# Performance work log

Hardware: AMD Instinct MI355X
Metric: run time of the kernel (lower is better)

## Reference

```python
import jax, jax.numpy as jnp
import numpy as np

B, C, T, N, KS = 16, 64, 64, 1024, 3

def setup_inputs() -> dict:
    key = jax.random.key(0)
    k1, k2, k3, k4 = jax.random.split(key, 4)
    x = jax.random.normal(k1, (B, C, T, N), dtype=jnp.float32)
    # scaled Chebyshev Laplacian terms; scale keeps activations sane
    Lk = jax.random.normal(k2, (KS, N, N), dtype=jnp.float32) / np.sqrt(N)
    # kaiming-uniform-ish init: bound = sqrt(6 / fan_in), fan_in = C*KS
    fan_in = C * KS
    bound_t = float(np.sqrt(6.0 / fan_in))
    theta = jax.random.uniform(k3, (C, C, KS), dtype=jnp.float32, minval=-bound_t, maxval=bound_t)
    bound_b = float(1.0 / np.sqrt(fan_in))
    b = jax.random.uniform(k4, (1, C, 1, 1), dtype=jnp.float32, minval=-bound_b, maxval=bound_b)
    return {"x": x, "Lk": Lk, "theta": theta, "b": b}

def reference(x, Lk, theta, b):
    # x: [b, c, t, n]; Lk: [ks, n, n]; theta: [c_in, c_out, ks]; b: [1, c, 1, 1]
    # Chebyshev graph contraction: aggregate over source nodes m for each order k
    x_c = jnp.einsum('knm,bitm->bitkn', Lk, x)          # [b, c, t, ks, n]
    # channel mixing over (c_in, ks)
    x_gc = jnp.einsum('iok,bitkn->botn', theta, x_c) + b  # [b, c, t, n]
    return jax.nn.relu(x_gc + x)
```

## Files before the change

### kernel.cpp

```cpp
#include <hip/hip_runtime.h>
#include <cstdint>
#include <cstddef>

typedef unsigned short u16;
typedef __attribute__((ext_vector_type(8))) short short8;
typedef __attribute__((ext_vector_type(4))) float f32x4;

#define B_DIM 16
#define C_DIM 64
#define T_DIM 64
#define N_DIM 1024
#define KS_DIM 3

#define BN 128
#define BK 32
#define NSTEP (N_DIM / BK)

__device__ __forceinline__ u16 f2bf(float f) {
  union { float f; uint32_t u; } v; v.f = f;
  uint32_t r = (v.u + 0x7FFFu + ((v.u >> 16) & 1u)) >> 16;
  return (u16)r;
}

__device__ __forceinline__ void gload_lds16(const void* g, void* l) {
  __builtin_amdgcn_global_load_lds(
      (const __attribute__((address_space(1))) void*)g,
      (__attribute__((address_space(3))) void*)l, 16, 0, 0);
}

__global__ void k_convert_lk(const float* __restrict__ Lk, u16* __restrict__ Lkb) {
  size_t idx = (size_t)blockIdx.x * blockDim.x + threadIdx.x;
  const float4* s = (const float4*)(Lk + idx * 8);
  float4 f0 = s[0], f1 = s[1];
  short8 h;
  h[0] = (short)f2bf(f0.x); h[1] = (short)f2bf(f0.y);
  h[2] = (short)f2bf(f0.z); h[3] = (short)f2bf(f0.w);
  h[4] = (short)f2bf(f1.x); h[5] = (short)f2bf(f1.y);
  h[6] = (short)f2bf(f1.z); h[7] = (short)f2bf(f1.w);
  *(short8*)(Lkb + idx * 8) = h;
}

__global__ void k_convert_theta(const float* __restrict__ th, u16* __restrict__ thT) {
  int f = blockIdx.x * blockDim.x + threadIdx.x;
  if (f < C_DIM * C_DIM * KS_DIM) {
    int o = f / 192, ik = f % 192, k = ik >> 6, i = ik & 63;
    thT[f] = f2bf(th[(i * 64 + o) * 3 + k]);
  }
}

__global__ __launch_bounds__(256, 3)
void k_main(const float* __restrict__ x, const u16* __restrict__ Lkb,
            const u16* __restrict__ thT, const float* __restrict__ bias,
            float* __restrict__ out) {
  __shared__ __align__(16) char smem[51200];
  u16* Ab = (u16*)smem;
  u16* Bb = (u16*)(smem + 4096);
  char* Zb = smem;

  const int tid = threadIdx.x;
  const int wv = tid >> 6;
  const int ln = tid & 63;
  const int lg = ln >> 4;
  const int l16 = ln & 15;

  const int bid = blockIdx.x;
  const int nt = bid & 7;
  const int slice = bid >> 3;
  const int bb = slice >> 6;
  const int tti = slice & 63;

  const f32x4 vzero = {0.f, 0.f, 0.f, 0.f};
  f32x4 acc[4][6];
#pragma unroll
  for (int a = 0; a < 4; ++a)
#pragma unroll
    for (int c = 0; c < 6; ++c) acc[a][c] = vzero;

  const int arow = tid >> 2, am = tid & 3;
  const float* a_src = x + (((size_t)bb * C_DIM + arow) * T_DIM + tti) * N_DIM + am * 8;

  for (int kk = 0; kk < NSTEP; ++kk) {
    if (kk) __syncthreads();
    {
      const float4* s = (const float4*)(a_src + kk * BK);
      float4 f0 = s[0], f1 = s[1];
      short8 h;
      h[0] = (short)f2bf(f0.x); h[1] = (short)f2bf(f0.y);
      h[2] = (short)f2bf(f0.z); h[3] = (short)f2bf(f0.w);
      h[4] = (short)f2bf(f1.x); h[5] = (short)f2bf(f1.y);
      h[6] = (short)f2bf(f1.z); h[7] = (short)f2bf(f1.w);
      *(short8*)(Ab + arow * BK + am * 8) = h;
    }
#pragma unroll
    for (int it = 0; it < 6; ++it) {
      int L = it * 256 + tid;
      int brow = L >> 2, msub = L & 3;
      int k = brow >> 7, nl = brow & 127;
      const u16* src = Lkb + ((size_t)(k * N_DIM + nt * BN + nl)) * N_DIM + kk * BK + msub * 8;
      char* dst = (char*)Bb + (size_t)(it * 256 + wv * 64) * 16;
      gload_lds16(src, dst);
    }
    __syncthreads();
    short8 af[4];
#pragma unroll
    for (int mi = 0; mi < 4; ++mi)
      af[mi] = *(const short8*)(Ab + (mi * 16 + l16) * BK + lg * 8);
#pragma unroll
    for (int ci = 0; ci < 6; ++ci) {
      int r = wv * 96 + ci * 16 + l16;
      short8 bf = *(const short8*)(Bb + r * BK + lg * 8);
#pragma unroll
      for (int mi = 0; mi < 4; ++mi)
        acc[mi][ci] = __builtin_amdgcn_mfma_f32_16x16x32_bf16(af[mi], bf, acc[mi][ci], 0, 0, 0);
    }
  }

  __syncthreads();
#pragma unroll
  for (int mi = 0; mi < 4; ++mi)
#pragma unroll
    for (int ci = 0; ci < 6; ++ci) {
      int c = wv * 96 + ci * 16 + l16;
      int k = c >> 7, nl = c & 127;
      int ib = mi * 16 + lg * 4;
      uint32_t p0 = (uint32_t)f2bf(acc[mi][ci][0]) | ((uint32_t)f2bf(acc[mi][ci][1]) << 16);
      uint32_t p1 = (uint32_t)f2bf(acc[mi][ci][2]) | ((uint32_t)f2bf(acc[mi][ci][3]) << 16);
      *(uint32_t*)(Zb + ((size_t)nl * 200 + k * 64 + ib) * 2) = p0;
      *(uint32_t*)(Zb + ((size_t)nl * 200 + k * 64 + ib + 2) * 2) = p1;
    }
  __syncthreads();

  f32x4 acc2[4][2];
#pragma unroll
  for (int a = 0; a < 4; ++a)
#pragma unroll
    for (int c = 0; c < 2; ++c) acc2[a][c] = vzero;

#pragma unroll
  for (int ks = 0; ks < 6; ++ks) {
    short8 af2[4];
#pragma unroll
    for (int mo = 0; mo < 4; ++mo) {
      int o = mo * 16 + l16;
      af2[mo] = *(const short8*)(thT + o * 192 + ks * 32 + lg * 8);
    }
#pragma unroll
    for (int cj = 0; cj < 2; ++cj) {
      int nl = wv * 32 + cj * 16 + l16;
      short8 bf = *(const short8*)(Zb + ((size_t)nl * 200 + ks * 32 + lg * 8) * 2);
#pragma unroll
      for (int mo = 0; mo < 4; ++mo)
        acc2[mo][cj] = __builtin_amdgcn_mfma_f32_16x16x32_bf16(af2[mo], bf, acc2[mo][cj], 0, 0, 0);
    }
  }

#pragma unroll
  for (int mo = 0; mo < 4; ++mo)
#pragma unroll
    for (int cj = 0; cj < 2; ++cj) {
      int nl = wv * 32 + cj * 16 + l16;
      int n = nt * BN + nl;
#pragma unroll
      for (int r = 0; r < 4; ++r) {
        int o = mo * 16 + lg * 4 + r;
        size_t oi = (((size_t)bb * C_DIM + o) * T_DIM + tti) * N_DIM + n;
        float v = acc2[mo][cj][r] + bias[o] + x[oi];
        out[oi] = v > 0.f ? v : 0.f;
      }
    }
}

extern "C" void kernel_launch(void* const* d_in, const int* in_sizes, int n_in,
                              void* d_out, int out_size, void* d_ws, size_t ws_size,
                              hipStream_t stream) {
  (void)in_sizes; (void)n_in; (void)out_size; (void)ws_size;
  const float* x     = (const float*)d_in[0];
  const float* Lk    = (const float*)d_in[1];
  const float* theta = (const float*)d_in[2];
  const float* bias  = (const float*)d_in[3];
  float* out = (float*)d_out;

  u16* Lkb = (u16*)d_ws;
  u16* thT = (u16*)((char*)d_ws + (size_t)KS_DIM * N_DIM * N_DIM * 2);

  k_convert_lk<<<KS_DIM * N_DIM * N_DIM / 8 / 256, 256, 0, stream>>>(Lk, Lkb);
  k_convert_theta<<<(C_DIM * C_DIM * KS_DIM + 255) / 256, 256, 0, stream>>>(theta, thT);
  k_main<<<B_DIM * T_DIM * (N_DIM / BN), 256, 0, stream>>>(x, Lkb, thT, bias, out);
}
```

Before: 1.020 ms.

## Double-buffer Lk tiles in LDS and XOR-swizzle A/B shared layouts

Moves the Lk (B) tile into two LDS buffers so the next k-step's async global-to-LDS loads are issued before the current step's MFMAs, overlapping memory with compute. The x (A) tile's fp32 loads for the next step are prefetched into registers and converted and stored after a barrier. An XOR swizzle on the 16-byte column chunk is applied to both A and B tiles to reduce LDS bank conflicts on fragment reads. Shared memory grows to 52KB and a second barrier per iteration is added, which may limit occupancy against the 3-blocks launch bound.

```diff
diff --git a/kernel.cpp b/kernel.cpp
--- a/kernel.cpp
+++ b/kernel.cpp
@@ -52,9 +52,10 @@
 void k_main(const float* __restrict__ x, const u16* __restrict__ Lkb,
             const u16* __restrict__ thT, const float* __restrict__ bias,
             float* __restrict__ out) {
-  __shared__ __align__(16) char smem[51200];
-  u16* Ab = (u16*)smem;
-  u16* Bb = (u16*)(smem + 4096);
+  __shared__ __align__(16) char smem[53248];
+  u16* Bb0 = (u16*)smem;
+  u16* Bb1 = (u16*)(smem + 24576);
+  u16* Ab  = (u16*)(smem + 49152);
   char* Zb = smem;
 
   const int tid = threadIdx.x;
@@ -78,44 +79,71 @@
 
   const int arow = tid >> 2, am = tid & 3;
   const float* a_src = x + (((size_t)bb * C_DIM + arow) * T_DIM + tti) * N_DIM + am * 8;
+  u16* a_dst = Ab + arow * BK + ((am ^ ((arow >> 1) & 3)) << 3);
+
+  const u16* b_srcb[6];
+  char* b_dst_off[6];
+#pragma unroll
+  for (int it = 0; it < 6; ++it) {
+    int L = it * 256 + tid;
+    int brow = L >> 2, msub = L & 3;
+    int k = brow >> 7, nl = brow & 127;
+    int msw = msub ^ ((brow >> 1) & 3);
+    b_srcb[it] = Lkb + ((size_t)(k * N_DIM + nt * BN + nl)) * N_DIM + (msw << 3);
+    b_dst_off[it] = (char*)((size_t)(it * 256 + wv * 64) * 16);
+  }
+
+  float4 a0 = *(const float4*)(a_src);
+  float4 a1 = *(const float4*)(a_src + 4);
+#pragma unroll
+  for (int it = 0; it < 6; ++it)
+    gload_lds16(b_srcb[it], (char*)Bb0 + (size_t)b_dst_off[it]);
+  {
+    short8 h;
+    h[0] = (short)f2bf(a0.x); h[1] = (short)f2bf(a0.y);
+    h[2] = (short)f2bf(a0.z); h[3] = (short)f2bf(a0.w);
+    h[4] = (short)f2bf(a1.x); h[5] = (short)f2bf(a1.y);
+    h[6] = (short)f2bf(a1.z); h[7] = (short)f2bf(a1.w);
+    *(short8*)a_dst = h;
+  }
+  __syncthreads();
 
   for (int kk = 0; kk < NSTEP; ++kk) {
-    if (kk) __syncthreads();
-    {
-      const float4* s = (const float4*)(a_src + kk * BK);
-      float4 f0 = s[0], f1 = s[1];
-      short8 h;
-      h[0] = (short)f2bf(f0.x); h[1] = (short)f2bf(f0.y);
-      h[2] = (short)f2bf(f0.z); h[3] = (short)f2bf(f0.w);
-      h[4] = (short)f2bf(f1.x); h[5] = (short)f2bf(f1.y);
-      h[6] = (short)f2bf(f1.z); h[7] = (short)f2bf(f1.w);
-      *(short8*)(Ab + arow * BK + am * 8) = h;
-    }
-#pragma unroll
-    for (int it = 0; it < 6; ++it) {
-      int L = it * 256 + tid;
-      int brow = L >> 2, msub = L & 3;
-      int k = brow >> 7, nl = brow & 127;
-      const u16* src = Lkb + ((size_t)(k * N_DIM + nt * BN + nl)) * N_DIM + kk * BK + msub * 8;
-      char* dst = (char*)Bb + (size_t)(it * 256 + wv * 64) * 16;
-      gload_lds16(src, dst);
-    }
-    __syncthreads();
+    u16* Bcur = (kk & 1) ? Bb1 : Bb0;
+    u16* Bnxt = (kk & 1) ? Bb0 : Bb1;
+    if (kk + 1 < NSTEP) {
+#pragma unroll
+      for (int it = 0; it < 6; ++it)
+        gload_lds16(b_srcb[it] + (kk + 1) * BK, (char*)Bnxt + (size_t)b_dst_off[it]);
+      a0 = *(const float4*)(a_src + (kk + 1) * BK);
+      a1 = *(const float4*)(a_src + (kk + 1) * BK + 4);
+    }
     short8 af[4];
 #pragma unroll
-    for (int mi = 0; mi < 4; ++mi)
-      af[mi] = *(const short8*)(Ab + (mi * 16 + l16) * BK + lg * 8);
+    for (int mi = 0; mi < 4; ++mi) {
+      int row = mi * 16 + l16;
+      af[mi] = *(const short8*)(Ab + row * BK + ((lg ^ ((row >> 1) & 3)) << 3));
+    }
 #pragma unroll
     for (int ci = 0; ci < 6; ++ci) {
       int r = wv * 96 + ci * 16 + l16;
-      short8 bf = *(const short8*)(Bb + r * BK + lg * 8);
+      short8 bfr = *(const short8*)(Bcur + r * BK + ((lg ^ ((r >> 1) & 3)) << 3));
 #pragma unroll
       for (int mi = 0; mi < 4; ++mi)
-        acc[mi][ci] = __builtin_amdgcn_mfma_f32_16x16x32_bf16(af[mi], bf, acc[mi][ci], 0, 0, 0);
-    }
-  }
-
-  __syncthreads();
+        acc[mi][ci] = __builtin_amdgcn_mfma_f32_16x16x32_bf16(af[mi], bfr, acc[mi][ci], 0, 0, 0);
+    }
+    __syncthreads();
+    if (kk + 1 < NSTEP) {
+      short8 h;
+      h[0] = (short)f2bf(a0.x); h[1] = (short)f2bf(a0.y);
+      h[2] = (short)f2bf(a0.z); h[3] = (short)f2bf(a0.w);
+      h[4] = (short)f2bf(a1.x); h[5] = (short)f2bf(a1.y);
+      h[6] = (short)f2bf(a1.z); h[7] = (short)f2bf(a1.w);
+      *(short8*)a_dst = h;
+    }
+    __syncthreads();
+  }
+
 #pragma unroll
   for (int mi = 0; mi < 4; ++mi)
 #pragma unroll
@@ -147,10 +175,10 @@
 #pragma unroll
     for (int cj = 0; cj < 2; ++cj) {
       int nl = wv * 32 + cj * 16 + l16;
-      short8 bf = *(const short8*)(Zb + ((size_t)nl * 200 + ks * 32 + lg * 8) * 2);
+      short8 bfr = *(const short8*)(Zb + ((size_t)nl * 200 + ks * 32 + lg * 8) * 2);
 #pragma unroll
       for (int mo = 0; mo < 4; ++mo)
-        acc2[mo][cj] = __builtin_amdgcn_mfma_f32_16x16x32_bf16(af2[mo], bf, acc2[mo][cj], 0, 0, 0);
+        acc2[mo][cj] = __builtin_amdgcn_mfma_f32_16x16x32_bf16(af2[mo], bfr, acc2[mo][cj], 0, 0, 0);
     }
   }
 
```

Measured after the change: 1.011 ms. No clear change (-0.8%).

## Retile main GEMM to 256x192 blocks with double-buffered swizzled LDS pipeline

Applied to the files above, without the earlier changes.

Each block now covers 4 time steps by 64 nodes (a 256-row by 192-column tile) with 8 waves, instead of one time step by 128 nodes with 4 waves. The inner K step grows to 64. A and B tiles are double-buffered in XOR-swizzled LDS, B comes in through async global-to-LDS loads, and x is prefetched two steps ahead in registers. Blocks are remapped for L2 locality and s_setprio is raised around the MFMA bursts. The goal is more reuse of the Lk tile across rows and hiding global load latency. The cost is 112KB of dynamic LDS per block, larger register pressure and lower occupancy.

```diff
diff --git a/kernel.cpp b/kernel.cpp
--- a/kernel.cpp
+++ b/kernel.cpp
@@ -11,17 +11,17 @@
 #define T_DIM 64
 #define N_DIM 1024
 #define KS_DIM 3
-
-#define BN 128
-#define BK 32
-#define NSTEP (N_DIM / BK)
+#define KSTEPS 16
+
 
 __device__ __forceinline__ u16 f2bf(float f) {
   union { float f; uint32_t u; } v; v.f = f;
   uint32_t r = (v.u + 0x7FFFu + ((v.u >> 16) & 1u)) >> 16;
   return (u16)r;
 }
-
+__device__ __forceinline__ uint32_t pk2(float a, float b) {
+  return (uint32_t)f2bf(a) | ((uint32_t)f2bf(b) << 16);
+}
 __device__ __forceinline__ void gload_lds16(const void* g, void* l) {
   __builtin_amdgcn_global_load_lds(
       (const __attribute__((address_space(1))) void*)g,
@@ -48,26 +48,20 @@
   }
 }
 
-__global__ __launch_bounds__(256, 3)
+__global__ __launch_bounds__(512, 2)
 void k_main(const float* __restrict__ x, const u16* __restrict__ Lkb,
             const u16* __restrict__ thT, const float* __restrict__ bias,
             float* __restrict__ out) {
-  __shared__ __align__(16) char smem[51200];
-  u16* Ab = (u16*)smem;
-  u16* Bb = (u16*)(smem + 4096);
-  char* Zb = smem;
+  extern __shared__ __align__(16) u16 smem[];
 
   const int tid = threadIdx.x;
-  const int wv = tid >> 6;
-  const int ln = tid & 63;
-  const int lg = ln >> 4;
-  const int l16 = ln & 15;
+  const int wv = tid >> 6, ln = tid & 63, lg = ln >> 4, l16 = ln & 15;
+  const int wr = wv >> 1, wc = wv & 1;
 
   const int bid = blockIdx.x;
-  const int nt = bid & 7;
-  const int slice = bid >> 3;
-  const int bb = slice >> 6;
-  const int tti = slice & 63;
+  const int work = ((bid & 7) << 9) + (bid >> 3);
+  const int sg = work >> 4, ng = work & 15;
+  const int bb = sg >> 4, t0 = (sg & 15) << 2;
 
   const f32x4 vzero = {0.f, 0.f, 0.f, 0.f};
   f32x4 acc[4][6];
@@ -76,81 +70,131 @@
 #pragma unroll
     for (int c = 0; c < 6; ++c) acc[a][c] = vzero;
 
-  const int arow = tid >> 2, am = tid & 3;
-  const float* a_src = x + (((size_t)bb * C_DIM + arow) * T_DIM + tti) * N_DIM + am * 8;
-
-  for (int kk = 0; kk < NSTEP; ++kk) {
-    if (kk) __syncthreads();
+  const int tr = tid >> 4;
+  const int fch = tid & 15;
+  const int ksb_a = fch >> 3;
+  const int g2 = (fch & 7) >> 1;
+  const int hf = fch & 1;
+  const int swa = (tr >> 1) & 3;
+  const float* a_base = x + (((size_t)bb * C_DIM + tr) * T_DIM + t0) * N_DIM + (fch << 2);
+#define AOFF(u) ((((u) & 1) * 32 * T_DIM + (((u) >> 1))) * N_DIM)
+  const int a_dst_c = ksb_a * 8192 + tr * 32 + ((g2 ^ swa) << 3) + (hf << 2);
+
+  const u16* b_src[3];
+  int b_dst_c[3];
+#pragma unroll
+  for (int it = 0; it < 3; ++it) {
+    int c = (it << 9) + tid;
+    int ksb = (c >= 768) ? 1 : 0;
+    int rem = c - ksb * 768;
+    int brow = rem >> 2, g = rem & 3;
+    int k = brow >> 6, nl = brow & 63;
+    int gs = g ^ ((brow >> 1) & 3);
+    b_src[it] = Lkb + ((size_t)(k * N_DIM + ng * 64 + nl)) * N_DIM + (ksb << 5) + (gs << 3);
+    b_dst_c[it] = ((it << 9) + (wv << 6)) << 3;
+  }
+
+  float4 q[8];
+
+#pragma unroll
+  for (int it = 0; it < 3; ++it)
+    gload_lds16(b_src[it], (char*)(smem + 32768) + ((size_t)b_dst_c[it] << 1));
+#pragma unroll
+  for (int u = 0; u < 8; ++u) q[u] = *(const float4*)(a_base + AOFF(u));
+  asm volatile("s_waitcnt vmcnt(0)" ::: "memory");
+#pragma unroll
+  for (int u = 0; u < 8; ++u) {
+    uint2 w; w.x = pk2(q[u].x, q[u].y); w.y = pk2(q[u].z, q[u].w);
+    *(uint2*)(smem + a_dst_c + u * 1024) = w;
+  }
+#pragma unroll
+  for (int u = 0; u < 8; ++u) q[u] = *(const float4*)(a_base + AOFF(u) + 64);
+  asm volatile("s_waitcnt lgkmcnt(0)" ::: "memory");
+  __builtin_amdgcn_s_barrier();
+
+  for (int kk = 0; kk < KSTEPS; ++kk) {
+    const int p = kk & 1, pn = p ^ 1;
+    const int wn = (kk + 1) & (KSTEPS - 1);
+    u16* Bn = smem + 32768 + pn * 12288;
+#pragma unroll
+    for (int it = 0; it < 3; ++it)
+      gload_lds16(b_src[it] + wn * 64, (char*)Bn + ((size_t)b_dst_c[it] << 1));
+    asm volatile("s_waitcnt vmcnt(3)" ::: "memory");
     {
-      const float4* s = (const float4*)(a_src + kk * BK);
-      float4 f0 = s[0], f1 = s[1];
-      short8 h;
-      h[0] = (short)f2bf(f0.x); h[1] = (short)f2bf(f0.y);
-      h[2] = (short)f2bf(f0.z); h[3] = (short)f2bf(f0.w);
-      h[4] = (short)f2bf(f1.x); h[5] = (short)f2bf(f1.y);
-      h[6] = (short)f2bf(f1.z); h[7] = (short)f2bf(f1.w);
-      *(short8*)(Ab + arow * BK + am * 8) = h;
-    }
-#pragma unroll
-    for (int it = 0; it < 6; ++it) {
-      int L = it * 256 + tid;
-      int brow = L >> 2, msub = L & 3;
-      int k = brow >> 7, nl = brow & 127;
-      const u16* src = Lkb + ((size_t)(k * N_DIM + nt * BN + nl)) * N_DIM + kk * BK + msub * 8;
-      char* dst = (char*)Bb + (size_t)(it * 256 + wv * 64) * 16;
-      gload_lds16(src, dst);
-    }
-    __syncthreads();
-    short8 af[4];
-#pragma unroll
-    for (int mi = 0; mi < 4; ++mi)
-      af[mi] = *(const short8*)(Ab + (mi * 16 + l16) * BK + lg * 8);
+      u16* ad = smem + pn * 16384 + a_dst_c;
+#pragma unroll
+      for (int u = 0; u < 8; ++u) {
+        uint2 w; w.x = pk2(q[u].x, q[u].y); w.y = pk2(q[u].z, q[u].w);
+        *(uint2*)(ad + u * 1024) = w;
+      }
+    }
+    {
+      const int w2 = (kk + 2) & (KSTEPS - 1);
+#pragma unroll
+      for (int u = 0; u < 8; ++u) q[u] = *(const float4*)(a_base + AOFF(u) + w2 * 64);
+    }
+    asm volatile("s_waitcnt lgkmcnt(0)" ::: "memory");
+    __builtin_amdgcn_s_barrier();
+    const u16* Ab = smem + p * 16384;
+    const u16* Bb = smem + 32768 + p * 12288;
+#pragma unroll
+    for (int ks = 0; ks < 2; ++ks) {
+      short8 af[4];
+#pragma unroll
+      for (int mi = 0; mi < 4; ++mi) {
+        int row = wr * 64 + mi * 16 + l16;
+        af[mi] = *(const short8*)(Ab + ks * 8192 + row * 32 + ((lg ^ ((row >> 1) & 3)) << 3));
+      }
+      __builtin_amdgcn_s_setprio(1);
+#pragma unroll
+      for (int ci = 0; ci < 6; ++ci) {
+        int brow = wc * 96 + ci * 16 + l16;
+        short8 bfr = *(const short8*)(Bb + ks * 6144 + brow * 32 + ((lg ^ ((brow >> 1) & 3)) << 3));
+#pragma unroll
+        for (int mi = 0; mi < 4; ++mi)
+          acc[mi][ci] = __builtin_amdgcn_mfma_f32_16x16x32_bf16(af[mi], bfr, acc[mi][ci], 0, 0, 0);
+      }
+      __builtin_amdgcn_s_setprio(0);
+    }
+    asm volatile("s_waitcnt lgkmcnt(0)" ::: "memory");
+    __builtin_amdgcn_s_barrier();
+  }
+
+  __syncthreads();
+
+#pragma unroll
+  for (int mi = 0; mi < 4; ++mi)
 #pragma unroll
     for (int ci = 0; ci < 6; ++ci) {
-      int r = wv * 96 + ci * 16 + l16;
-      short8 bf = *(const short8*)(Bb + r * BK + lg * 8);
-#pragma unroll
-      for (int mi = 0; mi < 4; ++mi)
-        acc[mi][ci] = __builtin_amdgcn_mfma_f32_16x16x32_bf16(af[mi], bf, acc[mi][ci], 0, 0, 0);
-    }
-  }
-
+      int c = wc * 96 + ci * 16 + l16;
+      int k = c >> 6, nl = c & 63;
+      int zrow = wr * 64 + nl;
+      int ib = mi * 16 + lg * 4;
+      u16* zp = smem + zrow * 200 + k * 64 + ib;
+      *(uint32_t*)zp = pk2(acc[mi][ci][0], acc[mi][ci][1]);
+      *(uint32_t*)(zp + 2) = pk2(acc[mi][ci][2], acc[mi][ci][3]);
+    }
   __syncthreads();
-#pragma unroll
-  for (int mi = 0; mi < 4; ++mi)
-#pragma unroll
-    for (int ci = 0; ci < 6; ++ci) {
-      int c = wv * 96 + ci * 16 + l16;
-      int k = c >> 7, nl = c & 127;
-      int ib = mi * 16 + lg * 4;
-      uint32_t p0 = (uint32_t)f2bf(acc[mi][ci][0]) | ((uint32_t)f2bf(acc[mi][ci][1]) << 16);
-      uint32_t p1 = (uint32_t)f2bf(acc[mi][ci][2]) | ((uint32_t)f2bf(acc[mi][ci][3]) << 16);
-      *(uint32_t*)(Zb + ((size_t)nl * 200 + k * 64 + ib) * 2) = p0;
-      *(uint32_t*)(Zb + ((size_t)nl * 200 + k * 64 + ib + 2) * 2) = p1;
-    }
-  __syncthreads();
 
   f32x4 acc2[4][2];
 #pragma unroll
   for (int a = 0; a < 4; ++a)
 #pragma unroll
     for (int c = 0; c < 2; ++c) acc2[a][c] = vzero;
-
+  const int s_e = wv >> 1, h_e = wv & 1;
 #pragma unroll
   for (int ks = 0; ks < 6; ++ks) {
     short8 af2[4];
 #pragma unroll
-    for (int mo = 0; mo < 4; ++mo) {
-      int o = mo * 16 + l16;
-      af2[mo] = *(const short8*)(thT + o * 192 + ks * 32 + lg * 8);
-    }
+    for (int mo = 0; mo < 4; ++mo)
+      af2[mo] = *(const short8*)(thT + (mo * 16 + l16) * 192 + ks * 32 + lg * 8);
 #pragma unroll
     for (int cj = 0; cj < 2; ++cj) {
-      int nl = wv * 32 + cj * 16 + l16;
-      short8 bf = *(const short8*)(Zb + ((size_t)nl * 200 + ks * 32 + lg * 8) * 2);
+      int nl = h_e * 32 + cj * 16 + l16;
+      short8 bfr = *(const short8*)(smem + (s_e * 64 + nl) * 200 + ks * 32 + lg * 8);
 #pragma unroll
       for (int mo = 0; mo < 4; ++mo)
-        acc2[mo][cj] = __builtin_amdgcn_mfma_f32_16x16x32_bf16(af2[mo], bf, acc2[mo][cj], 0, 0, 0);
+        acc2[mo][cj] = __builtin_amdgcn_mfma_f32_16x16x32_bf16(af2[mo], bfr, acc2[mo][cj], 0, 0, 0);
     }
   }
 
@@ -158,12 +202,12 @@
   for (int mo = 0; mo < 4; ++mo)
 #pragma unroll
     for (int cj = 0; cj < 2; ++cj) {
-      int nl = wv * 32 + cj * 16 + l16;
-      int n = nt * BN + nl;
+      int nl = h_e * 32 + cj * 16 + l16;
+      int n = ng * 64 + nl;
 #pragma unroll
       for (int r = 0; r < 4; ++r) {
         int o = mo * 16 + lg * 4 + r;
-        size_t oi = (((size_t)bb * C_DIM + o) * T_DIM + tti) * N_DIM + n;
+        size_t oi = (((size_t)bb * C_DIM + o) * T_DIM + t0 + s_e) * N_DIM + n;
         float v = acc2[mo][cj][r] + bias[o] + x[oi];
         out[oi] = v > 0.f ? v : 0.f;
       }
@@ -185,5 +229,7 @@
 
   k_convert_lk<<<KS_DIM * N_DIM * N_DIM / 8 / 256, 256, 0, stream>>>(Lk, Lkb);
   k_convert_theta<<<(C_DIM * C_DIM * KS_DIM + 255) / 256, 256, 0, stream>>>(theta, thT);
-  k_main<<<B_DIM * T_DIM * (N_DIM / BN), 256, 0, stream>>>(x, Lkb, thT, bias, out);
-}
+
+  hipFuncSetAttribute((const void*)k_main, hipFuncAttributeMaxDynamicSharedMemorySize, 114688);
+  k_main<<<B_DIM * T_DIM / 4 * 16, 512, 114688, stream>>>(x, Lkb, thT, bias, out);
+}
```

Result: slower. 1.300 ms (+27.5%).
